# Kernel tuning notes

Hardware: AMD Instinct MI355X
Metric: run time of the kernel (lower is better)

Reference implementation:

```python
import jax, jax.numpy as jnp
import numpy as np

MARGIN = 1.0
CURVATURE = 1.0
BOUNDARY_FACTOR = 2.0
MARGIN_THRESHOLD = 0.1
EPS = 1e-7


def setup_inputs() -> dict:
    key = jax.random.key(0)
    k1, k2 = jax.random.split(key)
    B, D = 4096, 128
    # scale so norms stay inside the unit Poincare ball (~0.57 on average)
    embeddings = jax.random.normal(k1, (B, D), dtype=jnp.float32) * 0.05
    labels = jax.random.randint(k2, (B,), 0, 64, dtype=jnp.int64)
    return {"embeddings": embeddings, "labels": labels}


def _poincare_distance_matrix(x, c):
    # d(x,y) = (1/sqrt(c)) * arccosh(1 + 2c||x-y||^2 / ((1-c||x||^2)(1-c||y||^2)))
    sq = jnp.sum(x * x, axis=-1)                       # [B]
    diff_sq = jnp.maximum(sq[:, None] + sq[None, :] - 2.0 * (x @ x.T), 0.0)
    denom = jnp.maximum((1.0 - c * sq[:, None]) * (1.0 - c * sq[None, :]), EPS)
    arg = 1.0 + 2.0 * c * diff_sq / denom
    return jnp.arccosh(jnp.maximum(arg, 1.0)) / jnp.sqrt(c)


def reference(embeddings, labels):
    B = embeddings.shape[0]
    distances = _poincare_distance_matrix(embeddings, CURVATURE)   # [B,B]

    same = labels[:, None] == labels[None, :]
    eye = jnp.eye(B, dtype=bool)
    positive_mask = same & ~eye
    negative_mask = ~same

    has_pos = jnp.any(positive_mask, axis=1)
    has_neg = jnp.any(negative_mask, axis=1)
    valid_anchor = has_pos & has_neg                               # [B]

    neg_inf = jnp.asarray(-jnp.inf, distances.dtype)
    hardest_pos = jnp.max(jnp.where(positive_mask, distances, neg_inf), axis=1)
    hardest_pos = jnp.where(has_pos, hardest_pos, 0.0)

    # adaptive margin (torch uses .item() -> detached from autograd)
    anchor_norm = jax.lax.stop_gradient(jnp.linalg.norm(embeddings, axis=-1))
    margin = jnp.maximum(MARGIN * (1.0 + BOUNDARY_FACTOR * anchor_norm),
                         MARGIN_THRESHOLD)                          # [B]

    pair_mask = valid_anchor[:, None] & negative_mask               # [B,B]
    raw = hardest_pos[:, None] - distances + margin[:, None]
    losses = jnp.maximum(raw, 0.0)

    total_triplets = jnp.sum(pair_mask)
    num_active = jnp.sum((raw > 0.0) & pair_mask)
    denom = jnp.maximum(total_triplets, 1).astype(losses.dtype)
    loss = jnp.sum(jnp.where(pair_mask, losses, 0.0)) / denom       # 'mean'

    active_ratio = num_active.astype(jnp.float32) / jnp.maximum(
        total_triplets.astype(jnp.float32), 1.0)
    pos_count = jnp.sum(positive_mask)
    mean_distance = jnp.where(
        pos_count > 0,
        jnp.sum(jnp.where(positive_mask, distances, 0.0))
        / jnp.maximum(pos_count, 1).astype(distances.dtype),
        0.0)

    return (loss, num_active, total_triplets, active_ratio, mean_distance)
```

## Files before the change

### kernel.cpp

```cpp
#include <hip/hip_runtime.h>
#include <hip/hip_bf16.h>
#include <math.h>

static constexpr int D        = 128;
static constexpr int NL       = 64;
static constexpr int NT       = 64;
static constexpr int LIDX_CAP = 512;

typedef __attribute__((ext_vector_type(8))) short  bf16x8;
typedef __attribute__((ext_vector_type(4))) float  f32x4;

__device__ __forceinline__ float wave_reduce_sum(float v) {
  #pragma unroll
  for (int o = 32; o; o >>= 1) v += __shfl_xor(v, o, 64);
  return v;
}

__device__ __forceinline__ float fast_acosh(float x) {
  float s = __builtin_amdgcn_sqrtf(fmaf(x, x, -1.0f));
  return __logf(x + s);
}

__device__ __forceinline__ unsigned short f2b(float x) {
  unsigned int u = __float_as_uint(x);
  unsigned int lsb = (u >> 16) & 1u;
  u += 0x7fffu + lsb;
  return (unsigned short)(u >> 16);
}
__device__ __forceinline__ float b2f(unsigned short u) {
  return __uint_as_float(((unsigned int)u) << 16);
}

__global__ __launch_bounds__(256) void kA(
    const float* __restrict__ emb, const int* __restrict__ lab,
    unsigned short* __restrict__ bfe, float* __restrict__ sq,
    float* __restrict__ vv, float* __restrict__ hpm,
    int* __restrict__ LC, float* __restrict__ plsum, int B) {
  const int t = threadIdx.x;
  const int bid = blockIdx.x;

  if (bid >= NL) {
    int w = t >> 6, lane = t & 63;
    int i = (bid - NL) * 4 + w;
    float2 v = reinterpret_cast<const float2*>(emb + (size_t)i * D)[lane];
    ushort2 bv = { f2b(v.x), f2b(v.y) };
    *reinterpret_cast<ushort2*>(&bfe[(size_t)i * D + 2 * lane]) = bv;
    float s = wave_reduce_sum(v.x * v.x + v.y * v.y);
    if (lane == 0) {
      sq[i] = s;
      vv[i] = 1.41421356237f / fmaxf(1.0f - s, 1e-6f);
    }
    return;
  }

  __shared__ unsigned short Al[NT][D + 8];
  __shared__ unsigned short Bl[NT][D + 8];
  __shared__ float rs[NT], rv[NT];
  __shared__ float cs[NT], cv[NT];
  __shared__ int   ridx[NT], cidx[NT];
  __shared__ int   lidx[LIDX_CAP];
  __shared__ int   parr[256];
  __shared__ float red[8];

  const int l = bid;
  const int wid = t >> 6, lane = t & 63;
  const int lr = lane & 15, lg = lane >> 4;

  int mc = 0;
  for (int i = t; i < B; i += 256) mc += (lab[i] == l) ? 1 : 0;
  parr[t] = mc;
  __syncthreads();
  for (int off = 1; off < 256; off <<= 1) {
    int v = (t >= off) ? parr[t - off] : 0;
    __syncthreads();
    parr[t] += v;
    __syncthreads();
  }
  const int c = parr[255];
  {
    int myoff = parr[t] - mc;
    for (int i = t; i < B; i += 256) {
      if (lab[i] == l) {
        if (myoff < LIDX_CAP) lidx[myoff] = i;
        ++myoff;
      }
    }
  }
  if (t == 0) { LC[l] = c; if (c == 0) plsum[l] = 0.0f; }
  if (c == 0) return;
  __syncthreads();

  const int  cc_    = min(c, LIDX_CAP);
  const bool validc = (c >= 2) && (c < B);
  float lsum = 0.0f;

  for (int i0 = 0; i0 < cc_; i0 += NT) {
    int ci = min(NT, cc_ - i0);
    __syncthreads();
    #pragma unroll
    for (int p = 0; p < 4; ++p) {
      int idx = t + p * 256;
      int r = idx >> 4, c16 = idx & 15;
      const float* src = emb + (size_t)lidx[i0 + min(r, ci - 1)] * D + c16 * 8;
      float4 a = *reinterpret_cast<const float4*>(src);
      float4 b = *reinterpret_cast<const float4*>(src + 4);
      ushort4 ua = { f2b(a.x), f2b(a.y), f2b(a.z), f2b(a.w) };
      ushort4 ub = { f2b(b.x), f2b(b.y), f2b(b.z), f2b(b.w) };
      *reinterpret_cast<ushort4*>(&Al[r][c16 * 8]) = ua;
      *reinterpret_cast<ushort4*>(&Al[r][c16 * 8 + 4]) = ub;
    }
    __syncthreads();
    {
      int r = t >> 2, q = t & 3;
      float s = 0.0f;
      #pragma unroll
      for (int i = 0; i < 4; ++i) {
        bf16x8 v8 = *reinterpret_cast<const bf16x8*>(&Al[r][q * 32 + i * 8]);
        #pragma unroll
        for (int j = 0; j < 8; ++j) {
          float x = b2f((unsigned short)v8[j]);
          s = fmaf(x, x, s);
        }
      }
      s += __shfl_xor(s, 1, 64);
      s += __shfl_xor(s, 2, 64);
      if (q == 0) {
        rs[r] = s;
        rv[r] = 1.41421356237f / fmaxf(1.0f - s, 1e-6f);
        ridx[r] = lidx[i0 + min(r, ci - 1)];
      }
    }

    float rmax[4] = {0.0f, 0.0f, 0.0f, 0.0f};

    for (int j0 = 0; j0 < cc_; j0 += NT) {
      int cj = min(NT, cc_ - j0);
      __syncthreads();
      #pragma unroll
      for (int p = 0; p < 4; ++p) {
        int idx = t + p * 256;
        int r = idx >> 4, c16 = idx & 15;
        const float* src = emb + (size_t)lidx[j0 + min(r, cj - 1)] * D + c16 * 8;
        float4 a = *reinterpret_cast<const float4*>(src);
        float4 b = *reinterpret_cast<const float4*>(src + 4);
        ushort4 ua = { f2b(a.x), f2b(a.y), f2b(a.z), f2b(a.w) };
        ushort4 ub = { f2b(b.x), f2b(b.y), f2b(b.z), f2b(b.w) };
        *reinterpret_cast<ushort4*>(&Bl[r][c16 * 8]) = ua;
        *reinterpret_cast<ushort4*>(&Bl[r][c16 * 8 + 4]) = ub;
      }
      __syncthreads();
      {
        int r = t >> 2, q = t & 3;
        float s = 0.0f;
        #pragma unroll
        for (int i = 0; i < 4; ++i) {
          bf16x8 v8 = *reinterpret_cast<const bf16x8*>(&Bl[r][q * 32 + i * 8]);
          #pragma unroll
          for (int j = 0; j < 8; ++j) {
            float x = b2f((unsigned short)v8[j]);
            s = fmaf(x, x, s);
          }
        }
        s += __shfl_xor(s, 1, 64);
        s += __shfl_xor(s, 2, 64);
        if (q == 0) {
          cs[r] = s;
          cv[r] = 1.41421356237f / fmaxf(1.0f - s, 1e-6f);
          cidx[r] = lidx[j0 + min(r, cj - 1)];
        }
      }
      __syncthreads();

      f32x4 dacc[4];
      #pragma unroll
      for (int n = 0; n < 4; ++n) dacc[n] = (f32x4){0.f, 0.f, 0.f, 0.f};
      #pragma unroll
      for (int kk = 0; kk < 4; ++kk) {
        bf16x8 a = *reinterpret_cast<const bf16x8*>(&Al[wid * 16 + lr][kk * 32 + lg * 8]);
        bf16x8 b[4];
        #pragma unroll
        for (int n = 0; n < 4; ++n)
          b[n] = *reinterpret_cast<const bf16x8*>(&Bl[n * 16 + lr][kk * 32 + lg * 8]);
        #pragma unroll
        for (int n = 0; n < 4; ++n)
          dacc[n] = __builtin_amdgcn_mfma_f32_16x16x32_bf16(a, b[n], dacc[n], 0, 0, 0);
      }

      int r0 = wid * 16 + lg * 4;
      #pragma unroll
      for (int n = 0; n < 4; ++n) {
        int ccn = n * 16 + lr;
        float sc = cs[ccn], vcv = cv[ccn];
        int   gj = cidx[ccn];
        #pragma unroll
        for (int g = 0; g < 4; ++g) {
          int rloc = r0 + g;
          if (rloc < ci && ccn < cj && ridx[rloc] != gj) {
            float diff = fmaxf(fmaf(-2.0f, dacc[n][g], rs[rloc] + sc), 0.0f);
            float arg  = fmaf(diff * rv[rloc], vcv, 1.0f);
            float d    = fast_acosh(arg);
            lsum += d;
            rmax[g] = fmaxf(rmax[g], d);
          }
        }
      }
    }

    int r0 = wid * 16 + lg * 4;
    #pragma unroll
    for (int g = 0; g < 4; ++g) {
      float v = rmax[g];
      v = fmaxf(v, __shfl_xor(v, 1, 64));
      v = fmaxf(v, __shfl_xor(v, 2, 64));
      v = fmaxf(v, __shfl_xor(v, 4, 64));
      v = fmaxf(v, __shfl_xor(v, 8, 64));
      int rloc = r0 + g;
      if (lr == 0 && rloc < ci) {
        float mg = fmaxf(fmaf(2.0f, __builtin_amdgcn_sqrtf(rs[rloc]), 1.0f), 0.1f);
        hpm[ridx[rloc]] = validc ? (v + mg) : -1e30f;
      }
    }
  }

  lsum = wave_reduce_sum(lsum);
  if (lane == 0) red[wid] = lsum;
  __syncthreads();
  if (t == 0) plsum[l] = (red[0] + red[1]) + (red[2] + red[3]);
}

__global__ __launch_bounds__(256) void k3_neg(
    const unsigned short* __restrict__ bfe, const int* __restrict__ lab,
    const float* __restrict__ sq, const float* __restrict__ vv,
    const float* __restrict__ hpm,
    float* __restrict__ part, int B, int G) {
  __shared__ unsigned short Al[NT][D + 8];
  __shared__ unsigned short Bl[NT][D + 8];
  __shared__ float rs[NT], rv[NT], rh[NT];
  __shared__ float cs[NT], cv[NT], ch[NT];
  __shared__ int   rl[NT], cl[NT];
  __shared__ float red[16];

  const int T2 = B / NT;
  const int ntile = T2 * (T2 + 1) / 2;
  const int t = threadIdx.x;
  const int wid = t >> 6, lane = t & 63;
  const int lr = lane & 15, lg = lane >> 4;
  const int bid = blockIdx.x;

  bf16x8 pre[8];
  float ps0 = 0, ps1 = 0, ps2 = 0;
  int   ps3 = 0;
  float nsum = 0.0f, nact = 0.0f;

  auto decode = [&](int tile, int& bi, int& bj) {
    float disc = (float)((2 * T2 + 1) * (2 * T2 + 1) - 8 * tile);
    int b = (int)(((float)(2 * T2 + 1) - __builtin_amdgcn_sqrtf(disc)) * 0.5f);
    b = max(0, min(b, T2 - 1));
    while (b * T2 - b * (b - 1) / 2 > tile) --b;
    while ((b + 1) * T2 - (b + 1) * b / 2 <= tile) ++b;
    bi = b;
    bj = b + (tile - (b * T2 - b * (b - 1) / 2));
  };

  auto load_tile = [&](int bi, int bj) {
    const unsigned short* ab = bfe + (size_t)bi * NT * D;
    const unsigned short* bb = bfe + (size_t)bj * NT * D;
    #pragma unroll
    for (int p = 0; p < 4; ++p) {
      int idx = t + p * 256;
      int r = idx >> 4, c16 = idx & 15;
      pre[p]     = reinterpret_cast<const bf16x8*>(ab + (size_t)r * D)[c16];
      pre[4 + p] = reinterpret_cast<const bf16x8*>(bb + (size_t)r * D)[c16];
    }
    if (t < NT) {
      int g = bi * NT + t;
      ps0 = sq[g]; ps1 = vv[g]; ps2 = hpm[g]; ps3 = lab[g];
    } else if (t < 2 * NT) {
      int g = bj * NT + (t - NT);
      ps0 = sq[g]; ps1 = vv[g]; ps2 = hpm[g]; ps3 = lab[g];
    }
  };

  int tile = bid;
  if (tile >= ntile) return;
  int bi, bj;
  decode(tile, bi, bj);
  float next_dsec = (bi == bj) ? 0.0f : 1.0f;
  load_tile(bi, bj);

  while (tile < ntile) {
    const float dsec = next_dsec;
    __syncthreads();
    #pragma unroll
    for (int p = 0; p < 4; ++p) {
      int idx = t + p * 256;
      int r = idx >> 4, c16 = idx & 15;
      *reinterpret_cast<bf16x8*>(&Al[r][c16 * 8]) = pre[p];
      *reinterpret_cast<bf16x8*>(&Bl[r][c16 * 8]) = pre[4 + p];
    }
    if (t < NT) {
      rs[t] = ps0; rv[t] = ps1; rh[t] = ps2; rl[t] = ps3;
    } else if (t < 2 * NT) {
      int r = t - NT;
      cs[r] = ps0; cv[r] = ps1; ch[r] = ps2; cl[r] = ps3;
    }
    int tile_next = tile + G;
    if (tile_next < ntile) {
      decode(tile_next, bi, bj);
      next_dsec = (bi == bj) ? 0.0f : 1.0f;
      load_tile(bi, bj);
    }
    __syncthreads();

    f32x4 dacc[4];
    #pragma unroll
    for (int n = 0; n < 4; ++n) dacc[n] = (f32x4){0.f, 0.f, 0.f, 0.f};
    #pragma unroll
    for (int kk = 0; kk < 4; ++kk) {
      bf16x8 a = *reinterpret_cast<const bf16x8*>(&Al[wid * 16 + lr][kk * 32 + lg * 8]);
      bf16x8 b[4];
      #pragma unroll
      for (int n = 0; n < 4; ++n)
        b[n] = *reinterpret_cast<const bf16x8*>(&Bl[n * 16 + lr][kk * 32 + lg * 8]);
      #pragma unroll
      for (int n = 0; n < 4; ++n)
        dacc[n] = __builtin_amdgcn_mfma_f32_16x16x32_bf16(a, b[n], dacc[n], 0, 0, 0);
    }

    int r0 = wid * 16 + lg * 4;
    f32x4 sr = *reinterpret_cast<const f32x4*>(&rs[r0]);
    f32x4 vr = *reinterpret_cast<const f32x4*>(&rv[r0]);
    f32x4 hr = *reinterpret_cast<const f32x4*>(&rh[r0]);
    int4  lm = *reinterpret_cast<const int4*>(&rl[r0]);
    int lmv[4] = { lm.x, lm.y, lm.z, lm.w };
    #pragma unroll
    for (int n = 0; n < 4; ++n) {
      int ccn = n * 16 + lr;
      float sc = cs[ccn], vcv = cv[ccn], hc = ch[ccn];
      int   lc = cl[ccn];
      #pragma unroll
      for (int g = 0; g < 4; ++g) {
        float diff = fmaxf(fmaf(-2.0f, dacc[n][g], sr[g] + sc), 0.0f);
        float arg  = fmaf(diff * vr[g], vcv, 1.0f);
        float d    = fast_acosh(arg);
        float r1   = hr[g] - d;
        float r2   = hc    - d;
        float neg  = (lmv[g] != lc) ? 1.0f : 0.0f;
        nsum += neg * (fmaxf(r1, 0.0f) + dsec * fmaxf(r2, 0.0f));
        nact += neg * ((r1 > 0.0f ? 1.0f : 0.0f) + dsec * (r2 > 0.0f ? 1.0f : 0.0f));
      }
    }
    tile = tile_next;
  }

  nsum = wave_reduce_sum(nsum);
  nact = wave_reduce_sum(nact);
  if (lane == 0) { red[wid] = nsum; red[8 + wid] = nact; }
  __syncthreads();
  if (t == 0) {
    part[2 * bid]     = (red[0] + red[1]) + (red[2] + red[3]);
    part[2 * bid + 1] = (red[8] + red[9]) + (red[10] + red[11]);
  }
}

__global__ __launch_bounds__(256) void k4_final(
    const float* __restrict__ part, int G,
    const int* __restrict__ LC, const float* __restrict__ plsum,
    float* __restrict__ out, int B) {
  __shared__ float sl[256], sa[256];
  __shared__ float fin[3];
  int t = threadIdx.x;
  float s = 0.0f, a = 0.0f;
  for (int i = t; i < G; i += 256) {
    s += part[2 * i];
    a += part[2 * i + 1];
  }
  sl[t] = s; sa[t] = a;
  __syncthreads();
  for (int o = 128; o; o >>= 1) {
    if (t < o) { sl[t] += sl[t + o]; sa[t] += sa[t + o]; }
    __syncthreads();
  }
  if (t < 64) {
    int   c  = LC[t];
    float cf = (float)c;
    float pc = cf * (cf - 1.0f);
    float tr = ((c >= 2) && (c < B)) ? cf * (float)(B - c) : 0.0f;
    float ps = plsum[t];
    pc = wave_reduce_sum(pc);
    tr = wave_reduce_sum(tr);
    ps = wave_reduce_sum(ps);
    if (t == 0) { fin[0] = pc; fin[1] = tr; fin[2] = ps; }
  }
  __syncthreads();
  if (t == 0) {
    float PC = fin[0], TR = fin[1], PS = fin[2];
    float den = fmaxf(TR, 1.0f);
    out[0] = sl[0] / den;
    out[1] = sa[0];
    out[2] = TR;
    out[3] = sa[0] / den;
    out[4] = (PC > 0.0f) ? PS / fmaxf(PC, 1.0f) : 0.0f;
  }
}

extern "C" void kernel_launch(void* const* d_in, const int* in_sizes, int n_in,
                              void* d_out, int out_size, void* d_ws, size_t ws_size,
                              hipStream_t stream) {
  const float* emb = (const float*)d_in[0];
  const int*   lab = (const int*)d_in[1];
  int B = in_sizes[1];

  int T = B / NT;
  int ntile = T * (T + 1) / 2;
  int G = 1024;
  if (G > ntile) G = ntile;

  unsigned short* bfe = (unsigned short*)d_ws;
  float* sq    = (float*)(bfe + (size_t)B * D);
  float* vv    = sq + B;
  float* hpm   = vv + B;
  int*   LC    = (int*)(hpm + B);
  float* plsum = (float*)(LC + NL);
  float* part  = plsum + NL;

  kA<<<NL + B / 4, 256, 0, stream>>>(emb, lab, bfe, sq, vv, hpm, LC, plsum, B);
  k3_neg<<<G, 256, 0, stream>>>(bfe, lab, sq, vv, hpm, part, B, G);
  k4_final<<<1, 256, 0, stream>>>(part, G, LC, plsum, (float*)d_out, B);
}
```

Before: 45.61 us.

## Use 128x128 upper-triangle tiles, one per 512-thread block, without persistent loop

The negative-pair kernel now covers 128x128 tiles of the upper triangle with 8 waves per block. Each wave computes a 64x32 sub-tile using 4x2 MFMA accumulators, which raises operand reuse from LDS. The persistent grid-stride loop with register prefetch is removed, so one block handles exactly one tile (528 blocks for B=4096). This halves global tile loads per output element, but the prefetch overlap is lost and the grid is smaller than the CU count times occupancy. LDS use grows to about 70 KB per block.

```diff
diff --git a/kernel.cpp b/kernel.cpp
--- a/kernel.cpp
+++ b/kernel.cpp
@@ -5,6 +5,7 @@
 static constexpr int D        = 128;
 static constexpr int NL       = 64;
 static constexpr int NT       = 64;
+static constexpr int NT2      = 128;
 static constexpr int LIDX_CAP = 512;
 
 typedef __attribute__((ext_vector_type(8))) short  bf16x8;
@@ -228,119 +229,92 @@
   if (t == 0) plsum[l] = (red[0] + red[1]) + (red[2] + red[3]);
 }
 
-__global__ __launch_bounds__(256) void k3_neg(
+__global__ __launch_bounds__(512) void k3_neg(
     const unsigned short* __restrict__ bfe, const int* __restrict__ lab,
     const float* __restrict__ sq, const float* __restrict__ vv,
     const float* __restrict__ hpm,
-    float* __restrict__ part, int B, int G) {
-  __shared__ unsigned short Al[NT][D + 8];
-  __shared__ unsigned short Bl[NT][D + 8];
-  __shared__ float rs[NT], rv[NT], rh[NT];
-  __shared__ float cs[NT], cv[NT], ch[NT];
-  __shared__ int   rl[NT], cl[NT];
+    float* __restrict__ part, int B) {
+  __shared__ unsigned short Al[NT2][D + 8];
+  __shared__ unsigned short Bl[NT2][D + 8];
+  __shared__ float rs[NT2], rv[NT2], rh[NT2];
+  __shared__ float cs[NT2], cv[NT2], ch[NT2];
+  __shared__ int   rl[NT2], cl[NT2];
   __shared__ float red[16];
 
-  const int T2 = B / NT;
-  const int ntile = T2 * (T2 + 1) / 2;
+  const int T2 = B / NT2;
   const int t = threadIdx.x;
   const int wid = t >> 6, lane = t & 63;
+  const int wr = wid >> 2, wc = wid & 3;
   const int lr = lane & 15, lg = lane >> 4;
   const int bid = blockIdx.x;
 
-  bf16x8 pre[8];
-  float ps0 = 0, ps1 = 0, ps2 = 0;
-  int   ps3 = 0;
+  float disc = (float)((2 * T2 + 1) * (2 * T2 + 1) - 8 * bid);
+  int bi = (int)(((float)(2 * T2 + 1) - __builtin_amdgcn_sqrtf(disc)) * 0.5f);
+  bi = max(0, min(bi, T2 - 1));
+  while (bi * T2 - bi * (bi - 1) / 2 > bid) --bi;
+  while ((bi + 1) * T2 - (bi + 1) * bi / 2 <= bid) ++bi;
+  int bj = bi + (bid - (bi * T2 - bi * (bi - 1) / 2));
+  const float dsec = (bi == bj) ? 0.0f : 1.0f;
+
+  const unsigned short* ab = bfe + (size_t)bi * NT2 * D;
+  const unsigned short* bb = bfe + (size_t)bj * NT2 * D;
+  #pragma unroll
+  for (int p = 0; p < 4; ++p) {
+    int idx = t + p * 512;
+    int r = idx >> 4, c16 = idx & 15;
+    bf16x8 va = reinterpret_cast<const bf16x8*>(ab + (size_t)r * D)[c16];
+    bf16x8 vb = reinterpret_cast<const bf16x8*>(bb + (size_t)r * D)[c16];
+    *reinterpret_cast<bf16x8*>(&Al[r][c16 * 8]) = va;
+    *reinterpret_cast<bf16x8*>(&Bl[r][c16 * 8]) = vb;
+  }
+  if (t < NT2) {
+    int g = bi * NT2 + t;
+    rs[t] = sq[g]; rv[t] = vv[g]; rh[t] = hpm[g]; rl[t] = lab[g];
+  } else if (t < 2 * NT2) {
+    int r = t - NT2, g = bj * NT2 + r;
+    cs[r] = sq[g]; cv[r] = vv[g]; ch[r] = hpm[g]; cl[r] = lab[g];
+  }
+  __syncthreads();
+
+  f32x4 dacc[4][2];
+  #pragma unroll
+  for (int m = 0; m < 4; ++m)
+    #pragma unroll
+    for (int n = 0; n < 2; ++n) dacc[m][n] = (f32x4){0.f, 0.f, 0.f, 0.f};
+
+  #pragma unroll
+  for (int kk = 0; kk < 4; ++kk) {
+    bf16x8 a[4], b[2];
+    #pragma unroll
+    for (int m = 0; m < 4; ++m)
+      a[m] = *reinterpret_cast<const bf16x8*>(&Al[wr * 64 + m * 16 + lr][kk * 32 + lg * 8]);
+    #pragma unroll
+    for (int n = 0; n < 2; ++n)
+      b[n] = *reinterpret_cast<const bf16x8*>(&Bl[wc * 32 + n * 16 + lr][kk * 32 + lg * 8]);
+    #pragma unroll
+    for (int m = 0; m < 4; ++m)
+      #pragma unroll
+      for (int n = 0; n < 2; ++n)
+        dacc[m][n] = __builtin_amdgcn_mfma_f32_16x16x32_bf16(a[m], b[n], dacc[m][n], 0, 0, 0);
+  }
+
   float nsum = 0.0f, nact = 0.0f;
-
-  auto decode = [&](int tile, int& bi, int& bj) {
-    float disc = (float)((2 * T2 + 1) * (2 * T2 + 1) - 8 * tile);
-    int b = (int)(((float)(2 * T2 + 1) - __builtin_amdgcn_sqrtf(disc)) * 0.5f);
-    b = max(0, min(b, T2 - 1));
-    while (b * T2 - b * (b - 1) / 2 > tile) --b;
-    while ((b + 1) * T2 - (b + 1) * b / 2 <= tile) ++b;
-    bi = b;
-    bj = b + (tile - (b * T2 - b * (b - 1) / 2));
-  };
-
-  auto load_tile = [&](int bi, int bj) {
-    const unsigned short* ab = bfe + (size_t)bi * NT * D;
-    const unsigned short* bb = bfe + (size_t)bj * NT * D;
-    #pragma unroll
-    for (int p = 0; p < 4; ++p) {
-      int idx = t + p * 256;
-      int r = idx >> 4, c16 = idx & 15;
-      pre[p]     = reinterpret_cast<const bf16x8*>(ab + (size_t)r * D)[c16];
-      pre[4 + p] = reinterpret_cast<const bf16x8*>(bb + (size_t)r * D)[c16];
-    }
-    if (t < NT) {
-      int g = bi * NT + t;
-      ps0 = sq[g]; ps1 = vv[g]; ps2 = hpm[g]; ps3 = lab[g];
-    } else if (t < 2 * NT) {
-      int g = bj * NT + (t - NT);
-      ps0 = sq[g]; ps1 = vv[g]; ps2 = hpm[g]; ps3 = lab[g];
-    }
-  };
-
-  int tile = bid;
-  if (tile >= ntile) return;
-  int bi, bj;
-  decode(tile, bi, bj);
-  float next_dsec = (bi == bj) ? 0.0f : 1.0f;
-  load_tile(bi, bj);
-
-  while (tile < ntile) {
-    const float dsec = next_dsec;
-    __syncthreads();
-    #pragma unroll
-    for (int p = 0; p < 4; ++p) {
-      int idx = t + p * 256;
-      int r = idx >> 4, c16 = idx & 15;
-      *reinterpret_cast<bf16x8*>(&Al[r][c16 * 8]) = pre[p];
-      *reinterpret_cast<bf16x8*>(&Bl[r][c16 * 8]) = pre[4 + p];
-    }
-    if (t < NT) {
-      rs[t] = ps0; rv[t] = ps1; rh[t] = ps2; rl[t] = ps3;
-    } else if (t < 2 * NT) {
-      int r = t - NT;
-      cs[r] = ps0; cv[r] = ps1; ch[r] = ps2; cl[r] = ps3;
-    }
-    int tile_next = tile + G;
-    if (tile_next < ntile) {
-      decode(tile_next, bi, bj);
-      next_dsec = (bi == bj) ? 0.0f : 1.0f;
-      load_tile(bi, bj);
-    }
-    __syncthreads();
-
-    f32x4 dacc[4];
-    #pragma unroll
-    for (int n = 0; n < 4; ++n) dacc[n] = (f32x4){0.f, 0.f, 0.f, 0.f};
-    #pragma unroll
-    for (int kk = 0; kk < 4; ++kk) {
-      bf16x8 a = *reinterpret_cast<const bf16x8*>(&Al[wid * 16 + lr][kk * 32 + lg * 8]);
-      bf16x8 b[4];
-      #pragma unroll
-      for (int n = 0; n < 4; ++n)
-        b[n] = *reinterpret_cast<const bf16x8*>(&Bl[n * 16 + lr][kk * 32 + lg * 8]);
-      #pragma unroll
-      for (int n = 0; n < 4; ++n)
-        dacc[n] = __builtin_amdgcn_mfma_f32_16x16x32_bf16(a, b[n], dacc[n], 0, 0, 0);
-    }
-
-    int r0 = wid * 16 + lg * 4;
+  #pragma unroll
+  for (int m = 0; m < 4; ++m) {
+    int r0 = wr * 64 + m * 16 + lg * 4;
     f32x4 sr = *reinterpret_cast<const f32x4*>(&rs[r0]);
     f32x4 vr = *reinterpret_cast<const f32x4*>(&rv[r0]);
     f32x4 hr = *reinterpret_cast<const f32x4*>(&rh[r0]);
     int4  lm = *reinterpret_cast<const int4*>(&rl[r0]);
     int lmv[4] = { lm.x, lm.y, lm.z, lm.w };
     #pragma unroll
-    for (int n = 0; n < 4; ++n) {
-      int ccn = n * 16 + lr;
+    for (int n = 0; n < 2; ++n) {
+      int ccn = wc * 32 + n * 16 + lr;
       float sc = cs[ccn], vcv = cv[ccn], hc = ch[ccn];
       int   lc = cl[ccn];
       #pragma unroll
       for (int g = 0; g < 4; ++g) {
-        float diff = fmaxf(fmaf(-2.0f, dacc[n][g], sr[g] + sc), 0.0f);
+        float diff = fmaxf(fmaf(-2.0f, dacc[m][n][g], sr[g] + sc), 0.0f);
         float arg  = fmaf(diff * vr[g], vcv, 1.0f);
         float d    = fast_acosh(arg);
         float r1   = hr[g] - d;
@@ -350,7 +324,6 @@
         nact += neg * ((r1 > 0.0f ? 1.0f : 0.0f) + dsec * (r2 > 0.0f ? 1.0f : 0.0f));
       }
     }
-    tile = tile_next;
   }
 
   nsum = wave_reduce_sum(nsum);
@@ -358,8 +331,11 @@
   if (lane == 0) { red[wid] = nsum; red[8 + wid] = nact; }
   __syncthreads();
   if (t == 0) {
-    part[2 * bid]     = (red[0] + red[1]) + (red[2] + red[3]);
-    part[2 * bid + 1] = (red[8] + red[9]) + (red[10] + red[11]);
+    float S = 0.0f, A = 0.0f;
+    #pragma unroll
+    for (int w = 0; w < 8; ++w) { S += red[w]; A += red[8 + w]; }
+    part[2 * bid]     = S;
+    part[2 * bid + 1] = A;
   }
 }
 
@@ -411,10 +387,8 @@
   const int*   lab = (const int*)d_in[1];
   int B = in_sizes[1];
 
-  int T = B / NT;
-  int ntile = T * (T + 1) / 2;
-  int G = 1024;
-  if (G > ntile) G = ntile;
+  int T2 = B / NT2;
+  int ntile = T2 * (T2 + 1) / 2;
 
   unsigned short* bfe = (unsigned short*)d_ws;
   float* sq    = (float*)(bfe + (size_t)B * D);
@@ -425,6 +399,6 @@
   float* part  = plsum + NL;
 
   kA<<<NL + B / 4, 256, 0, stream>>>(emb, lab, bfe, sq, vv, hpm, LC, plsum, B);
-  k3_neg<<<G, 256, 0, stream>>>(bfe, lab, sq, vv, hpm, part, B, G);
-  k4_final<<<1, 256, 0, stream>>>(part, G, LC, plsum, (float*)d_out, B);
-}
+  k3_neg<<<ntile, 512, 0, stream>>>(bfe, lab, sq, vv, hpm, part, B);
+  k4_final<<<1, 256, 0, stream>>>(part, ntile, LC, plsum, (float*)d_out, B);
+}
```

Result: faster. 44.19 us (median of 2 runs) (-3.1%).
